# Optimization experiments

Measured on AMD Instinct MI355X. Metric: run time of the kernel, lower is better.

## Reference

```python
import jax, jax.numpy as jnp
import numpy as np

D_MODEL = 1024
N_SH = 16            # sub-heads per branch
N_BR = 4             # branches
H_TOT = N_BR * N_SH  # 64 total heads
DH = D_MODEL // N_SH # 64 head dim
BRANCH_CONFIGS = [(16, 0), (128, 16), (128, 0), (512, 144)]


def rms_norm(x):
    eps = jnp.finfo(x.dtype).eps
    return x * jax.lax.rsqrt(jnp.mean(x * x, axis=-1, keepdims=True) + eps)


def rope(x):
    # x: [B, H, T, Dh]; non-standard RoPE: even/odd split, halves concatenated
    T, Dh = x.shape[2], x.shape[3]
    inv_freq = 1.0 / (10000.0 ** (jnp.arange(0, Dh, 2, dtype=jnp.float32) / Dh))
    freqs = jnp.arange(T, dtype=jnp.float32)[:, None] * inv_freq[None, :]  # [T, Dh/2]
    cos = jnp.cos(freqs)[None, None]
    sin = jnp.sin(freqs)[None, None]
    x1 = x[..., 0::2]
    x2 = x[..., 1::2]
    return jnp.concatenate([-x2 * sin + x1 * cos, x1 * sin + x2 * cos], axis=-1)


def setup_inputs() -> dict:
    key = jax.random.key(0)
    ks = jax.random.split(key, 12)
    B, T, C = 2, 1024, D_MODEL
    s = 0.02
    return {
        "X": jax.random.normal(ks[0], (B, T, C), jnp.float32),
        "WQ": jax.random.normal(ks[1], (C, H_TOT * DH), jnp.float32) * s,
        "bQ": jax.random.normal(ks[2], (H_TOT * DH,), jnp.float32) * s,
        "WK": jax.random.normal(ks[3], (C, C), jnp.float32) * s,
        "bK": jax.random.normal(ks[4], (C,), jnp.float32) * s,
        "WV": jax.random.normal(ks[5], (C, H_TOT * DH), jnp.float32) * s,
        "bV": jax.random.normal(ks[6], (H_TOT * DH,), jnp.float32) * s,
        "WO": jax.random.normal(ks[7], (C, C), jnp.float32) * s,
        "bO": jax.random.normal(ks[8], (C,), jnp.float32) * s,
        "sink_scalars": jax.random.normal(ks[9], (H_TOT,), jnp.float32) * s,
        "v_nulls": jax.random.normal(ks[10], (H_TOT, DH), jnp.float32) * s,
    }


def reference(X, WQ, bQ, WK, bK, WV, bV, WO, bO, sink_scalars, v_nulls):
    B, T, C = X.shape
    # projections -> [B, H, T, Dh]
    q = (X @ WQ + bQ).reshape(B, T, H_TOT, DH).transpose(0, 2, 1, 3)
    q = rope(rms_norm(q))
    v = (X @ WV + bV).reshape(B, T, H_TOT, DH).transpose(0, 2, 1, 3)
    k = rope((X @ WK + bK).reshape(B, T, N_SH, DH).transpose(0, 2, 1, 3))
    k = jnp.tile(k, (1, N_BR, 1, 1))  # [B, H_TOT, T, Dh]

    # KMax scores with key self-norm denominator
    scores = jnp.einsum('bhqd,bhkd->bhqk', q, k)
    denom = jnp.sqrt(jnp.sum(k * k, axis=-1))[:, :, None, :]  # [B,H,1,T]
    w = scores / denom

    # banded masks per branch; note: off-band logits become 0 (NOT -inf) -> exp(0)=1 in softmax
    idx = jnp.arange(T)
    dist = idx[:, None] - idx[None, :]  # query - key
    bmasks = jnp.stack([((dist >= g) & (dist < h)).astype(w.dtype)
                        for (h, g) in BRANCH_CONFIGS], axis=0)  # [N_BR,T,T]
    full_mask = jnp.repeat(bmasks, N_SH, axis=0)[None]  # [1,H_TOT,T,T] (band subset of tril)
    w = w * full_mask

    # learnable tanh sink logit per head, concatenated as extra column
    sinks = jnp.broadcast_to(jnp.tanh(sink_scalars).reshape(1, H_TOT, 1, 1), (B, H_TOT, T, 1))
    probs = jax.nn.softmax(jnp.concatenate([w, sinks], axis=-1), axis=-1)

    out = jnp.einsum('bhqk,bhkd->bhqd', probs[..., :T], v)
    out = out + probs[..., T:] * v_nulls.reshape(1, H_TOT, 1, DH)

    # [B,H_TOT,T,Dh] -> [B,N_BR,T,C]
    ctx = out.reshape(B, N_BR, N_SH, T, DH).transpose(0, 1, 3, 2, 4).reshape(B, N_BR, T, C)
    y = ctx @ WO + bO
    return y.mean(axis=1)
```

## Files before the change

kernel.cpp:

```cpp
#include <hip/hip_runtime.h>
#include <hip/hip_bf16.h>
#include <math.h>

#define T_SEQ 1024
#define LOG2_10000 13.287712379549449f

typedef unsigned short u16;
typedef unsigned int u32;
typedef __attribute__((ext_vector_type(8))) short bf16x8;
typedef __attribute__((ext_vector_type(4))) float f32x4;

__device__ __forceinline__ void gload16(const u16* g, const u16* s) {
  __builtin_amdgcn_global_load_lds(
      (const __attribute__((address_space(1))) void*)g,
      (__attribute__((address_space(3))) void*)s, 16, 0, 0);
}

__device__ __forceinline__ u16 f2bf(float x) {
  __hip_bfloat16 h = __float2bfloat16(x);
  return *reinterpret_cast<u16*>(&h);
}
__device__ __forceinline__ float bf2f(u16 x) {
  __hip_bfloat16 h = *reinterpret_cast<__hip_bfloat16*>(&x);
  return __bfloat162float(h);
}

__device__ __forceinline__ float wave_sum64(float v) {
  v += __shfl_xor(v, 1, 64);
  v += __shfl_xor(v, 2, 64);
  v += __shfl_xor(v, 4, 64);
  v += __shfl_xor(v, 8, 64);
  v += __shfl_xor(v, 16, 64);
  v += __shfl_xor(v, 32, 64);
  return v;
}

__device__ __forceinline__ void transpose_step(
    const float* __restrict__ W, u16* __restrict__ Wt, int N, int nbx,
    int local, int t, float (*tile)[33]) {
  int bx = local % nbx, by = local / nbx;
  int n0 = bx * 32, k0 = by * 32;
  int r = t >> 3, c4 = (t & 7) * 4;
  float4 v = *reinterpret_cast<const float4*>(&W[(size_t)(k0 + r) * N + n0 + c4]);
  tile[r][c4 + 0] = v.x;
  tile[r][c4 + 1] = v.y;
  tile[r][c4 + 2] = v.z;
  tile[r][c4 + 3] = v.w;
  __syncthreads();
  u16 o[4];
#pragma unroll
  for (int i = 0; i < 4; ++i) o[i] = f2bf(tile[c4 + i][r]);
  *reinterpret_cast<uint2*>(&Wt[(size_t)(n0 + r) * 1024 + k0 + c4]) =
      *reinterpret_cast<const uint2*>(o);
}

__global__ __launch_bounds__(256) void prep_kernel(
    const float* __restrict__ X, const float* __restrict__ WQ,
    const float* __restrict__ WK, const float* __restrict__ WV,
    const float* __restrict__ WO, const float* __restrict__ bQ,
    const float* __restrict__ bV, const float* __restrict__ bK,
    u16* __restrict__ Xb, u16* __restrict__ WQVKt, u16* __restrict__ WOt,
    float* __restrict__ bQVK, float* __restrict__ ctab, float* __restrict__ stab)
{
  __shared__ float tile[32][33];
  const int blk = blockIdx.x, t = threadIdx.x;
  if (blk < 128) {
    int id = blk * 256 + t;
    int tt = id >> 5, p = id & 31;
    float invf = exp2f(-LOG2_10000 * (float)(2 * p) * (1.0f / 64.0f));
    float ang = (float)tt * invf;
    float sn, cs;
    sincosf(ang, &sn, &cs);
    ctab[id] = cs;
    stab[id] = sn;
  } else if (blk < 1152) {
    int i = (blk - 128) * 256 + t;
    float4 a = reinterpret_cast<const float4*>(X)[2 * i];
    float4 b = reinterpret_cast<const float4*>(X)[2 * i + 1];
    u16 o[8] = {f2bf(a.x), f2bf(a.y), f2bf(a.z), f2bf(a.w),
                f2bf(b.x), f2bf(b.y), f2bf(b.z), f2bf(b.w)};
    reinterpret_cast<uint4*>(Xb)[i] = *reinterpret_cast<const uint4*>(o);
  } else if (blk < 5248) {
    transpose_step(WQ, WQVKt, 4096, 128, blk - 1152, t, tile);
  } else if (blk < 9344) {
    transpose_step(WV, WQVKt + (size_t)4096 * 1024, 4096, 128, blk - 5248, t, tile);
  } else if (blk < 10368) {
    transpose_step(WK, WQVKt + (size_t)8192 * 1024, 1024, 32, blk - 9344, t, tile);
  } else if (blk < 11392) {
    transpose_step(WO, WOt, 1024, 32, blk - 10368, t, tile);
  } else {
    int id = (blk - 11392) * 256 + t;
    if (id < 9216)
      bQVK[id] = (id < 4096) ? bQ[id] : (id < 8192) ? bV[id - 4096] : bK[id - 8192];
  }
}

__global__ __launch_bounds__(256) void vsum_part_kernel(
    const u16* __restrict__ QVbf, float* __restrict__ part) {
  int blk = blockIdx.x;
  int b = blk >> 6, ch = blk & 63;
  const u16* base = QVbf + (size_t)(b * 1024 + ch * 16) * 8192 + 4096;
#pragma unroll
  for (int g = 0; g < 2; ++g) {
    int c0 = (threadIdx.x + g * 256) * 8;
    float s[8] = {0.f, 0.f, 0.f, 0.f, 0.f, 0.f, 0.f, 0.f};
#pragma unroll 4
    for (int r = 0; r < 16; ++r) {
      bf16x8 v = *reinterpret_cast<const bf16x8*>(&base[(size_t)r * 8192 + c0]);
#pragma unroll
      for (int e = 0; e < 8; ++e) s[e] += bf2f((u16)v[e]);
    }
    float* dst = &part[(size_t)blk * 4096 + c0];
#pragma unroll
    for (int e = 0; e < 8; ++e) dst[e] = s[e];
  }
}

__global__ __launch_bounds__(256) void vsum_reduce_kernel(
    const float* __restrict__ part, float* __restrict__ Vsum) {
  int id = blockIdx.x * 256 + threadIdx.x;
  int b = id >> 12, n = id & 4095;
  float s = 0.f;
#pragma unroll 8
  for (int ch = 0; ch < 64; ++ch) s += part[(size_t)(b * 64 + ch) * 4096 + n];
  Vsum[id] = s;
}

__global__ __launch_bounds__(512, 1) void gemm_qv_kernel(
    const u16* __restrict__ Ab, const u16* __restrict__ Bt,
    const float* __restrict__ bias, u16* __restrict__ Cqv)
{
  __shared__ __align__(16) u16 sA[4][256 * 32];
  __shared__ __align__(16) u16 sB[4][256 * 32];

  const int tid = threadIdx.x;
  const int lane = tid & 63;
  const int w = tid >> 6;
  const int wm = w >> 2, wn = w & 3;
  const int l15 = lane & 15, l4 = lane >> 4;

  const int orig = blockIdx.x;
  const int xcd = orig & 7, j = orig >> 3;
  const int by = (xcd >> 2) * 4 + (j >> 3);
  const int bx = (xcd & 3) * 8 + (j & 7);
  const int m0 = by * 256, n0 = bx * 256;

  const int r0s = tid >> 2,         c0s = tid & 3;
  const int r1s = (512 + tid) >> 2, c1s = (512 + tid) & 3;
  const int sc0 = c0s ^ ((r0s >> 1) & 3);
  const int sc1 = c1s ^ ((r1s >> 1) & 3);
  const u16* aA0 = Ab + (size_t)(m0 + r0s) * 1024 + 8 * sc0;
  const u16* aA1 = Ab + (size_t)(m0 + r1s) * 1024 + 8 * sc1;
  const u16* aB0 = Bt + (size_t)(n0 + r0s) * 1024 + 8 * sc0;
  const u16* aB1 = Bt + (size_t)(n0 + r1s) * 1024 + 8 * sc1;

  const int cp = l4 ^ ((l15 >> 1) & 3);

  f32x4 acc[8][4];
#pragma unroll
  for (int i = 0; i < 8; ++i)
#pragma unroll
    for (int jn = 0; jn < 4; ++jn) acc[i][jn] = (f32x4){0.f, 0.f, 0.f, 0.f};

#define STAGE32(t)                                                             \
  {                                                                            \
    const int sl = (t) & 3;                                                    \
    const int ko = (t) * 32;                                                   \
    gload16(aA0 + ko, &sA[sl][tid * 8]);                                       \
    gload16(aA1 + ko, &sA[sl][4096 + tid * 8]);                                \
    gload16(aB0 + ko, &sB[sl][tid * 8]);                                       \
    gload16(aB1 + ko, &sB[sl][4096 + tid * 8]);                                \
  }

  STAGE32(0);
  STAGE32(1);
#pragma unroll 1
  for (int t = 0; t < 32; ++t) {
    if (t + 2 < 32) {
      STAGE32(t + 2);
      asm volatile("s_waitcnt vmcnt(8)" ::: "memory");
    } else if (t + 1 < 32) {
      asm volatile("s_waitcnt vmcnt(4)" ::: "memory");
    } else {
      asm volatile("s_waitcnt vmcnt(0)" ::: "memory");
    }
    __builtin_amdgcn_sched_barrier(0);
    __builtin_amdgcn_s_barrier();
    __builtin_amdgcn_sched_barrier(0);

    const u16* tA = sA[t & 3];
    const u16* tB = sB[t & 3];

    bf16x8 bf[4];
#pragma unroll
    for (int n = 0; n < 4; ++n) {
      int row = wn * 64 + n * 16 + l15;
      bf[n] = *reinterpret_cast<const bf16x8*>(&tB[row * 32 + cp * 8]);
    }
    bf16x8 af[8];
#pragma unroll
    for (int m = 0; m < 8; ++m) {
      int row = wm * 128 + m * 16 + l15;
      af[m] = *reinterpret_cast<const bf16x8*>(&tA[row * 32 + cp * 8]);
    }
    __builtin_amdgcn_s_setprio(1);
#pragma unroll
    for (int m = 0; m < 8; ++m)
#pragma unroll
      for (int n = 0; n < 4; ++n)
        acc[m][n] = __builtin_amdgcn_mfma_f32_16x16x32_bf16(
            af[m], bf[n], acc[m][n], 0, 0, 0);
    __builtin_amdgcn_s_setprio(0);
  }
#undef STAGE32

#pragma unroll
  for (int n = 0; n < 4; ++n) {
    int col = n0 + wn * 64 + n * 16 + l15;
    float bv = bias[col];
#pragma unroll
    for (int mf = 0; mf < 8; ++mf) {
#pragma unroll
      for (int r = 0; r < 4; ++r) {
        int row = m0 + wm * 128 + mf * 16 + l4 * 4 + r;
        Cqv[(size_t)row * 8192 + col] = f2bf(acc[mf][n][r] + bv);
      }
    }
  }
}

template <bool BF16OUT>
__global__ __launch_bounds__(256) void gemm64_kernel(
    const u16* __restrict__ Ab, const u16* __restrict__ Bt,
    const float* __restrict__ bias, void* __restrict__ Cv,
    int M, int N, int K)
{
  __shared__ __align__(16) u16 sA[64 * 32];
  __shared__ __align__(16) u16 sB[64 * 32];
  const int tid = threadIdx.x;
  const int lane = tid & 63;
  const int wv = tid >> 6;
  const int wm = wv >> 1, wn = wv & 1;
  const int l15 = lane & 15, l4 = lane >> 4;
  const int m0 = blockIdx.y * 64, n0 = blockIdx.x * 64;

  f32x4 acc[2][2];
#pragma unroll
  for (int i = 0; i < 2; ++i)
#pragma unroll
    for (int j = 0; j < 2; ++j) acc[i][j] = (f32x4){0.f, 0.f, 0.f, 0.f};

  const int r0 = tid >> 2, kc = tid & 3;
  const u16* a_src = Ab + (size_t)(m0 + r0) * K + kc * 8;
  const u16* b_src = Bt + (size_t)(n0 + r0) * K + kc * 8;
  u16* dA = sA + (size_t)wv * 512;
  u16* dB = sB + (size_t)wv * 512;
  const int kcol = l4 * 8;

  for (int k0 = 0; k0 < K; k0 += 32) {
    __syncthreads();
    gload16(a_src + k0, dA);
    gload16(b_src + k0, dB);
    __syncthreads();
    bf16x8 af[2], bfv[2];
#pragma unroll
    for (int mi = 0; mi < 2; ++mi)
      af[mi] = *reinterpret_cast<const bf16x8*>(&sA[(wm * 32 + mi * 16 + l15) * 32 + kcol]);
#pragma unroll
    for (int ni = 0; ni < 2; ++ni)
      bfv[ni] = *reinterpret_cast<const bf16x8*>(&sB[(wn * 32 + ni * 16 + l15) * 32 + kcol]);
#pragma unroll
    for (int mi = 0; mi < 2; ++mi)
#pragma unroll
      for (int ni = 0; ni < 2; ++ni)
        acc[mi][ni] = __builtin_amdgcn_mfma_f32_16x16x32_bf16(
            af[mi], bfv[ni], acc[mi][ni], 0, 0, 0);
  }

#pragma unroll
  for (int mi = 0; mi < 2; ++mi)
#pragma unroll
    for (int ni = 0; ni < 2; ++ni) {
      int col = n0 + wn * 32 + ni * 16 + l15;
      float bv = bias[col];
#pragma unroll
      for (int r = 0; r < 4; ++r) {
        int row = m0 + wm * 32 + mi * 16 + l4 * 4 + r;
        float val = acc[mi][ni][r] + bv;
        size_t idx = (size_t)row * N + col;
        if (BF16OUT) ((u16*)Cv)[idx] = f2bf(val);
        else ((float*)Cv)[idx] = val;
      }
    }
}

__global__ __launch_bounds__(256) void qk_transform_kernel(
    u16* __restrict__ QVbf, u16* __restrict__ Kbf,
    const float* __restrict__ ctab, const float* __restrict__ stab)
{
  const int rid  = blockIdx.x * 8 + (threadIdx.x >> 5);
  const int lane = threadIdx.x & 63;
  const int p    = lane & 31;
  const int gb   = lane & 32;

  u16* row;
  int t;
  const bool isQ = rid < 131072;
  if (isQ) {
    int h = rid & 63, bt = rid >> 6;
    t = bt & 1023;
    row = QVbf + (size_t)bt * 8192 + h * 64;
  } else {
    int r2 = rid - 131072;
    int hsL = r2 & 15, bt = r2 >> 4;
    t = bt & 1023;
    row = Kbf + (size_t)bt * 1024 + hsL * 64;
  }

  u32 v = reinterpret_cast<const u32*>(row)[p];
  float x1 = bf2f((u16)v), x2 = bf2f((u16)(v >> 16));
  float cs = ctab[t * 32 + p], sn = stab[t * 32 + p];

  float o_lo, o_hi;
  if (isQ) {
    float ss = x1 * x1 + x2 * x2;
    ss += __shfl_xor(ss, 1, 64);
    ss += __shfl_xor(ss, 2, 64);
    ss += __shfl_xor(ss, 4, 64);
    ss += __shfl_xor(ss, 8, 64);
    ss += __shfl_xor(ss, 16, 64);
    float rs = rsqrtf(ss * (1.0f / 64.0f) + 1.1920929e-7f);
    float xn1 = x1 * rs, xn2 = x2 * rs;
    o_lo = xn1 * cs - xn2 * sn;
    o_hi = xn1 * sn + xn2 * cs;
  } else {
    float xr1 = x1 * cs - x2 * sn;
    float xr2 = x1 * sn + x2 * cs;
    float ss = xr1 * xr1 + xr2 * xr2;
    ss += __shfl_xor(ss, 1, 64);
    ss += __shfl_xor(ss, 2, 64);
    ss += __shfl_xor(ss, 4, 64);
    ss += __shfl_xor(ss, 8, 64);
    ss += __shfl_xor(ss, 16, 64);
    float rs = rsqrtf(ss);
    o_lo = xr1 * rs;
    o_hi = xr2 * rs;
  }

  int m = (2 * p) & 31;
  float slo0 = __shfl(o_lo, gb + m, 64);
  float slo1 = __shfl(o_lo, gb + m + 1, 64);
  float shi0 = __shfl(o_hi, gb + m, 64);
  float shi1 = __shfl(o_hi, gb + m + 1, 64);
  float e0 = (p < 16) ? slo0 : shi0;
  float e1 = (p < 16) ? slo1 : shi1;
  reinterpret_cast<u32*>(row)[p] = (u32)f2bf(e0) | ((u32)f2bf(e1) << 16);
}

__global__ __launch_bounds__(256) void attn_mfma_kernel(
    const u16* __restrict__ Qv, const u16* __restrict__ Kb,
    const float* __restrict__ Vsum, const float* __restrict__ sink,
    const float* __restrict__ vnull, u16* __restrict__ mctxb)
{
  __shared__ __align__(16) u16 sQ[64 * 64];
  __shared__ __align__(16) u16 sK[2][64 * 64];
  __shared__ __align__(16) u16 sVt[2][64 * 64];
  __shared__ __align__(16) u16 sP[64 * 64];

  int blk = blockIdx.x;
  blk = (blk & 7) * 64 + (blk >> 3);
  const int qt  = blk & 15;
  const int hs  = (blk >> 4) & 15;
  const int b   = blk >> 8;
  const int qt0 = qt * 64;

  const int tid  = threadIdx.x;
  const int lane = tid & 63;
  const int wv   = tid >> 6;
  const int l15  = lane & 15;
  const int l4   = lane >> 4;
  const int qr0  = tid >> 3, qi0 = tid & 7;
  const int qr1  = qr0 + 32;
  const int vjp  = tid & 31, vdg = tid >> 5;
  const int qrow = wv * 16 + l15;

  constexpr int HCFG[4] = {16, 128, 128, 512};
  constexpr int GCFG[4] = {0, 16, 0, 144};

  f32x4 macc[4];
#pragma unroll
  for (int i = 0; i < 4; ++i) macc[i] = (f32x4){0.f, 0.f, 0.f, 0.f};

#pragma unroll 1
  for (int br = 0; br < 4; ++br) {
    const int h = br * 16 + hs;
    const int hmax = HCFG[br], g = GCFG[br];
    int klo = qt0 - (hmax - 1); if (klo < 0) klo = 0;
    int khi = qt0 + 63 - g;     if (khi > 1023) khi = 1023;
    const int nc = (khi >= klo) ? ((khi - klo) / 64 + 1) : 0;

    gload16(Qv + (size_t)(b * 1024 + qt0 + qr0) * 8192 + h * 64 + 8 * (qi0 ^ (qr0 & 7)),
            sQ + (size_t)wv * 512);
    gload16(Qv + (size_t)(b * 1024 + qt0 + qr1) * 8192 + h * 64 + 8 * (qi0 ^ (qr1 & 7)),
            sQ + 2048 + (size_t)wv * 512);
    bf16x8 va, vb;
    if (nc > 0) {
      int ja0 = klo + qr0; if (ja0 > 1023) ja0 = 1023;
      int ja1 = klo + qr1; if (ja1 > 1023) ja1 = 1023;
      gload16(Kb + (size_t)(b * 1024 + ja0) * 1024 + hs * 64 + 8 * (qi0 ^ (qr0 & 7)),
              sK[0] + (size_t)wv * 512);
      gload16(Kb + (size_t)(b * 1024 + ja1) * 1024 + hs * 64 + 8 * (qi0 ^ (qr1 & 7)),
              sK[0] + 2048 + (size_t)wv * 512);
      int jva = klo + 2 * vjp, jvb = jva + 1;
      if (jva > 1023) jva = 1023;
      if (jvb > 1023) jvb = 1023;
      va = *reinterpret_cast<const bf16x8*>(
          &Qv[(size_t)(b * 1024 + jva) * 8192 + 4096 + h * 64 + vdg * 8]);
      vb = *reinterpret_cast<const bf16x8*>(
          &Qv[(size_t)(b * 1024 + jvb) * 8192 + 4096 + h * 64 + vdg * 8]);
    }
    asm volatile("s_waitcnt vmcnt(0)" ::: "memory");
    __builtin_amdgcn_sched_barrier(0);
    if (nc > 0) {
#pragma unroll
      for (int e = 0; e < 8; ++e) {
        int d = vdg * 8 + e;
        u32 pack = (u32)(u16)va[e] | ((u32)(u16)vb[e] << 16);
        *reinterpret_cast<u32*>(
            (char*)sVt[0] + d * 128 + ((4 * vjp) ^ ((d & 7) << 4))) = pack;
      }
    }
    asm volatile("s_waitcnt lgkmcnt(0)" ::: "memory");
    __builtin_amdgcn_sched_barrier(0);
    __builtin_amdgcn_s_barrier();

    bf16x8 afQ[2];
#pragma unroll
    for (int kh = 0; kh < 2; ++kh) {
      int cs = (4 * kh + l4) ^ (l15 & 7);
      afQ[kh] = *reinterpret_cast<const bf16x8*>(&sQ[qrow * 64 + cs * 8]);
    }

    f32x4 outv[4];
#pragma unroll
    for (int i = 0; i < 4; ++i) outv[i] = (f32x4){0.f, 0.f, 0.f, 0.f};
    float zacc[4] = {0.f, 0.f, 0.f, 0.f};

    int buf = 0;
#pragma unroll 1
    for (int c = 0; c < nc; ++c) {
      const int j0 = klo + c * 64;
      const bool nxt = (c + 1 < nc);
      if (nxt) {
        int j0n = j0 + 64;
        int ja0 = j0n + qr0; if (ja0 > 1023) ja0 = 1023;
        int ja1 = j0n + qr1; if (ja1 > 1023) ja1 = 1023;
        gload16(Kb + (size_t)(b * 1024 + ja0) * 1024 + hs * 64 + 8 * (qi0 ^ (qr0 & 7)),
                sK[buf ^ 1] + (size_t)wv * 512);
        gload16(Kb + (size_t)(b * 1024 + ja1) * 1024 + hs * 64 + 8 * (qi0 ^ (qr1 & 7)),
                sK[buf ^ 1] + 2048 + (size_t)wv * 512);
        int jva = j0n + 2 * vjp, jvb = jva + 1;
        if (jva > 1023) jva = 1023;
        if (jvb > 1023) jvb = 1023;
        va = *reinterpret_cast<const bf16x8*>(
            &Qv[(size_t)(b * 1024 + jva) * 8192 + 4096 + h * 64 + vdg * 8]);
        vb = *reinterpret_cast<const bf16x8*>(
            &Qv[(size_t)(b * 1024 + jvb) * 8192 + 4096 + h * 64 + vdg * 8]);
      }
      f32x4 sfr[4];
#pragma unroll
      for (int jt = 0; jt < 4; ++jt) {
        int krow = jt * 16 + l15;
        f32x4 acc = (f32x4){0.f, 0.f, 0.f, 0.f};
#pragma unroll
        for (int kh = 0; kh < 2; ++kh) {
          int cs = (4 * kh + l4) ^ (l15 & 7);
          bf16x8 bk = *reinterpret_cast<const bf16x8*>(&sK[buf][krow * 64 + cs * 8]);
          acc = __builtin_amdgcn_mfma_f32_16x16x32_bf16(afQ[kh], bk, acc, 0, 0, 0);
        }
        sfr[jt] = acc;
      }
#pragma unroll
      for (int jt = 0; jt < 4; ++jt) {
        int jloc = jt * 16 + l15;
        int jabs = j0 + jloc;
#pragma unroll
        for (int r = 0; r < 4; ++r) {
          int q_r = wv * 16 + l4 * 4 + r;
          int dist = (qt0 + q_r) - jabs;
          bool inband = (dist >= g) & (dist < hmax) & (jabs < 1024);
          float pv = inband ? (__expf(sfr[jt][r]) - 1.0f) : 0.0f;
          zacc[r] += pv;
          *reinterpret_cast<u16*>(
              (char*)sP + q_r * 128 + ((2 * jloc) ^ ((q_r & 7) << 4))) = f2bf(pv);
        }
      }
      asm volatile("s_waitcnt lgkmcnt(0)" ::: "memory");
      __builtin_amdgcn_sched_barrier(0);
      bf16x8 afP[2];
#pragma unroll
      for (int kh = 0; kh < 2; ++kh) {
        int cs = (4 * kh + l4) ^ (l15 & 7);
        afP[kh] = *reinterpret_cast<const bf16x8*>(&sP[qrow * 64 + cs * 8]);
      }
#pragma unroll
      for (int dt = 0; dt < 4; ++dt) {
        int drow = dt * 16 + l15;
#pragma unroll
        for (int kh = 0; kh < 2; ++kh) {
          int cs = (4 * kh + l4) ^ (l15 & 7);
          bf16x8 bv = *reinterpret_cast<const bf16x8*>(&sVt[buf][drow * 64 + cs * 8]);
          outv[dt] = __builtin_amdgcn_mfma_f32_16x16x32_bf16(afP[kh], bv, outv[dt], 0, 0, 0);
        }
      }
      if (nxt) {
#pragma unroll
        for (int e = 0; e < 8; ++e) {
          int d = vdg * 8 + e;
          u32 pack = (u32)(u16)va[e] | ((u32)(u16)vb[e] << 16);
          *reinterpret_cast<u32*>(
              (char*)sVt[buf ^ 1] + d * 128 + ((4 * vjp) ^ ((d & 7) << 4))) = pack;
        }
      }
      asm volatile("s_waitcnt vmcnt(0) lgkmcnt(0)" ::: "memory");
      __builtin_amdgcn_sched_barrier(0);
      __builtin_amdgcn_s_barrier();
      buf ^= 1;
    }

#pragma unroll
    for (int r = 0; r < 4; ++r) {
      zacc[r] += __shfl_xor(zacc[r], 1, 64);
      zacc[r] += __shfl_xor(zacc[r], 2, 64);
      zacc[r] += __shfl_xor(zacc[r], 4, 64);
      zacc[r] += __shfl_xor(zacc[r], 8, 64);
    }
    float es = __expf(tanhf(sink[h]));
#pragma unroll
    for (int dt = 0; dt < 4; ++dt) {
      int d = dt * 16 + l15;
      float vs = Vsum[(size_t)b * 4096 + h * 64 + d];
      float vn = vnull[h * 64 + d];
#pragma unroll
      for (int r = 0; r < 4; ++r) {
        float invZ = 1.0f / (1024.0f + zacc[r] + es);
        macc[dt][r] += (outv[dt][r] + vs + es * vn) * invZ;
      }
    }
  }

#pragma unroll
  for (int dt = 0; dt < 4; ++dt) {
#pragma unroll
    for (int r = 0; r < 4; ++r) {
      int q_r = wv * 16 + l4 * 4 + r;
      mctxb[(size_t)(b * 1024 + qt0 + q_r) * 1024 + hs * 64 + dt * 16 + l15] =
          f2bf(0.25f * macc[dt][r]);
    }
  }
}

extern "C" void kernel_launch(void* const* d_in, const int* in_sizes, int n_in,
                              void* d_out, int out_size, void* d_ws, size_t ws_size,
                              hipStream_t stream) {
  (void)in_sizes; (void)n_in; (void)out_size; (void)ws_size;
  const float* X    = (const float*)d_in[0];
  const float* WQ   = (const float*)d_in[1];
  const float* bQ   = (const float*)d_in[2];
  const float* WK   = (const float*)d_in[3];
  const float* bK   = (const float*)d_in[4];
  const float* WV   = (const float*)d_in[5];
  const float* bV   = (const float*)d_in[6];
  const float* WO   = (const float*)d_in[7];
  const float* bO   = (const float*)d_in[8];
  const float* sink = (const float*)d_in[9];
  const float* vnul = (const float*)d_in[10];
  float* Y = (float*)d_out;

  char* p = (char*)d_ws;
  u16*   Xb    = (u16*)p;   p += (size_t)2048 * 1024 * 2;
  u16*   WQVKt = (u16*)p;   p += (size_t)9216 * 1024 * 2;
  u16*   WOt   = (u16*)p;   p += (size_t)1024 * 1024 * 2;
  u16*   QVbf  = (u16*)p;   p += (size_t)2048 * 8192 * 2;
  u16*   Kbf   = (u16*)p;   p += (size_t)2048 * 1024 * 2;
  u16*   mctxb = (u16*)p;   p += (size_t)2048 * 1024 * 2;
  float* Vsum  = (float*)p; p += (size_t)2 * 4096 * 4;
  float* vpart = (float*)p; p += (size_t)128 * 4096 * 4;
  float* bQVK  = (float*)p; p += (size_t)9216 * 4;
  float* ctab  = (float*)p; p += (size_t)32768 * 4;
  float* stab  = (float*)p; p += (size_t)32768 * 4;

  dim3 blk(256);
  prep_kernel<<<11428, blk, 0, stream>>>(X, WQ, WK, WV, WO, bQ, bV, bK,
                                         Xb, WQVKt, WOt, bQVK, ctab, stab);

  gemm_qv_kernel<<<256, dim3(512), 0, stream>>>(Xb, WQVKt, bQVK, QVbf);
  gemm64_kernel<true><<<dim3(16, 32), blk, 0, stream>>>(
      Xb, WQVKt + (size_t)8192 * 1024, bQVK + 8192, Kbf, 2048, 1024, 1024);

  vsum_part_kernel<<<128, blk, 0, stream>>>(QVbf, vpart);
  vsum_reduce_kernel<<<32, blk, 0, stream>>>(vpart, Vsum);

  qk_transform_kernel<<<20480, blk, 0, stream>>>(QVbf, Kbf, ctab, stab);

  attn_mfma_kernel<<<512, blk, 0, stream>>>(QVbf, Kbf, Vsum, sink, vnul, mctxb);

  gemm64_kernel<false><<<dim3(16, 32), blk, 0, stream>>>(mctxb, WOt, bO, Y, 2048, 1024, 1024);
}
```

Before: 139.7 us.

## Fuse Q RMSNorm+RoPE into QV GEMM epilogue and double-buffer gemm64

Q normalization and rotary embedding move into the QV GEMM epilogue, computed from accumulators with lane shuffles, so the standalone transform now handles only K rows. This avoids a separate read-modify-write pass over the 2048x4096 bf16 Q region. The small 64x64 GEMM also gains a double-buffered LDS pipeline, prefetching the next K-slice while computing the current one. The cost is a heavier epilogue with extra shuffles and table loads, plus reliance on manual waitcnt/barrier ordering.

```diff
diff --git a/kernel.cpp b/kernel.cpp
--- a/kernel.cpp
+++ b/kernel.cpp
@@ -23,16 +23,6 @@
 __device__ __forceinline__ float bf2f(u16 x) {
   __hip_bfloat16 h = *reinterpret_cast<__hip_bfloat16*>(&x);
   return __bfloat162float(h);
-}
-
-__device__ __forceinline__ float wave_sum64(float v) {
-  v += __shfl_xor(v, 1, 64);
-  v += __shfl_xor(v, 2, 64);
-  v += __shfl_xor(v, 4, 64);
-  v += __shfl_xor(v, 8, 64);
-  v += __shfl_xor(v, 16, 64);
-  v += __shfl_xor(v, 32, 64);
-  return v;
 }
 
 __device__ __forceinline__ void transpose_step(
@@ -128,7 +118,8 @@
 
 __global__ __launch_bounds__(512, 1) void gemm_qv_kernel(
     const u16* __restrict__ Ab, const u16* __restrict__ Bt,
-    const float* __restrict__ bias, u16* __restrict__ Cqv)
+    const float* __restrict__ bias, u16* __restrict__ Cqv,
+    const float* __restrict__ ctab, const float* __restrict__ stab)
 {
   __shared__ __align__(16) u16 sA[4][256 * 32];
   __shared__ __align__(16) u16 sB[4][256 * 32];
@@ -214,16 +205,60 @@
   }
 #undef STAGE32
 
-#pragma unroll
-  for (int n = 0; n < 4; ++n) {
-    int col = n0 + wn * 64 + n * 16 + l15;
-    float bv = bias[col];
+  float bv4[4];
+#pragma unroll
+  for (int n = 0; n < 4; ++n) bv4[n] = bias[n0 + wn * 64 + n * 16 + l15];
+
+  if (bx < 16) {
+    const int srcl = (lane & 0x30) | ((2 * l15) & 15);
+    const bool hi8 = (l15 >= 8);
 #pragma unroll
     for (int mf = 0; mf < 8; ++mf) {
 #pragma unroll
       for (int r = 0; r < 4; ++r) {
         int row = m0 + wm * 128 + mf * 16 + l4 * 4 + r;
-        Cqv[(size_t)row * 8192 + col] = f2bf(acc[mf][n][r] + bv);
+        int tt = row & 1023;
+        float v0 = acc[mf][0][r] + bv4[0];
+        float v1 = acc[mf][1][r] + bv4[1];
+        float v2 = acc[mf][2][r] + bv4[2];
+        float v3 = acc[mf][3][r] + bv4[3];
+        float ss = v0 * v0 + v1 * v1 + v2 * v2 + v3 * v3;
+        ss += __shfl_xor(ss, 1, 64);
+        ss += __shfl_xor(ss, 2, 64);
+        ss += __shfl_xor(ss, 4, 64);
+        ss += __shfl_xor(ss, 8, 64);
+        float rs = rsqrtf(ss * (1.0f / 64.0f) + 1.1920929e-7f);
+        float x0 = v0 * rs, x1f = v1 * rs, x2f = v2 * rs, x3f = v3 * rs;
+        float tc0 = ctab[tt * 32 + l15],      ts0 = stab[tt * 32 + l15];
+        float tc1 = ctab[tt * 32 + 16 + l15], ts1 = stab[tt * 32 + 16 + l15];
+        float e0a = __shfl(x0,  srcl, 64),     e0b = __shfl(x1f, srcl, 64);
+        float o0a = __shfl(x0,  srcl + 1, 64), o0b = __shfl(x1f, srcl + 1, 64);
+        float e1a = __shfl(x2f, srcl, 64),     e1b = __shfl(x3f, srcl, 64);
+        float o1a = __shfl(x2f, srcl + 1, 64), o1b = __shfl(x3f, srcl + 1, 64);
+        float X1_0 = hi8 ? e0b : e0a, X2_0 = hi8 ? o0b : o0a;
+        float X1_1 = hi8 ? e1b : e1a, X2_1 = hi8 ? o1b : o1a;
+        u16 out0 = f2bf(X1_0 * tc0 - X2_0 * ts0);
+        u16 out1 = f2bf(X1_1 * tc1 - X2_1 * ts1);
+        u16 out2 = f2bf(X1_0 * ts0 + X2_0 * tc0);
+        u16 out3 = f2bf(X1_1 * ts1 + X2_1 * tc1);
+        size_t base_ = (size_t)row * 8192 + n0 + wn * 64 + l15;
+        Cqv[base_ + 0]  = out0;
+        Cqv[base_ + 16] = out1;
+        Cqv[base_ + 32] = out2;
+        Cqv[base_ + 48] = out3;
+      }
+    }
+  } else {
+#pragma unroll
+    for (int n = 0; n < 4; ++n) {
+      int col = n0 + wn * 64 + n * 16 + l15;
+#pragma unroll
+      for (int mf = 0; mf < 8; ++mf) {
+#pragma unroll
+        for (int r = 0; r < 4; ++r) {
+          int row = m0 + wm * 128 + mf * 16 + l4 * 4 + r;
+          Cqv[(size_t)row * 8192 + col] = f2bf(acc[mf][n][r] + bv4[n]);
+        }
       }
     }
   }
@@ -235,8 +270,8 @@
     const float* __restrict__ bias, void* __restrict__ Cv,
     int M, int N, int K)
 {
-  __shared__ __align__(16) u16 sA[64 * 32];
-  __shared__ __align__(16) u16 sB[64 * 32];
+  __shared__ __align__(16) u16 sA[2][64 * 32];
+  __shared__ __align__(16) u16 sB[2][64 * 32];
   const int tid = threadIdx.x;
   const int lane = tid & 63;
   const int wv = tid >> 6;
@@ -253,22 +288,33 @@
   const int r0 = tid >> 2, kc = tid & 3;
   const u16* a_src = Ab + (size_t)(m0 + r0) * K + kc * 8;
   const u16* b_src = Bt + (size_t)(n0 + r0) * K + kc * 8;
-  u16* dA = sA + (size_t)wv * 512;
-  u16* dB = sB + (size_t)wv * 512;
   const int kcol = l4 * 8;
 
-  for (int k0 = 0; k0 < K; k0 += 32) {
-    __syncthreads();
-    gload16(a_src + k0, dA);
-    gload16(b_src + k0, dB);
-    __syncthreads();
+  gload16(a_src, &sA[0][(size_t)wv * 512]);
+  gload16(b_src, &sB[0][(size_t)wv * 512]);
+
+  const int niter = K >> 5;
+#pragma unroll 1
+  for (int it = 0; it < niter; ++it) {
+    const int buf = it & 1;
+    __builtin_amdgcn_s_barrier();
+    if (it + 1 < niter) {
+      gload16(a_src + (it + 1) * 32, &sA[buf ^ 1][(size_t)wv * 512]);
+      gload16(b_src + (it + 1) * 32, &sB[buf ^ 1][(size_t)wv * 512]);
+      asm volatile("s_waitcnt vmcnt(2)" ::: "memory");
+    } else {
+      asm volatile("s_waitcnt vmcnt(0)" ::: "memory");
+    }
+    __builtin_amdgcn_sched_barrier(0);
     bf16x8 af[2], bfv[2];
 #pragma unroll
     for (int mi = 0; mi < 2; ++mi)
-      af[mi] = *reinterpret_cast<const bf16x8*>(&sA[(wm * 32 + mi * 16 + l15) * 32 + kcol]);
+      af[mi] = *reinterpret_cast<const bf16x8*>(
+          &sA[buf][(wm * 32 + mi * 16 + l15) * 32 + kcol]);
 #pragma unroll
     for (int ni = 0; ni < 2; ++ni)
-      bfv[ni] = *reinterpret_cast<const bf16x8*>(&sB[(wn * 32 + ni * 16 + l15) * 32 + kcol]);
+      bfv[ni] = *reinterpret_cast<const bf16x8*>(
+          &sB[buf][(wn * 32 + ni * 16 + l15) * 32 + kcol]);
 #pragma unroll
     for (int mi = 0; mi < 2; ++mi)
 #pragma unroll
@@ -294,58 +340,33 @@
     }
 }
 
-__global__ __launch_bounds__(256) void qk_transform_kernel(
-    u16* __restrict__ QVbf, u16* __restrict__ Kbf,
-    const float* __restrict__ ctab, const float* __restrict__ stab)
+__global__ __launch_bounds__(256) void k_transform_kernel(
+    u16* __restrict__ Kbf, const float* __restrict__ ctab,
+    const float* __restrict__ stab)
 {
   const int rid  = blockIdx.x * 8 + (threadIdx.x >> 5);
   const int lane = threadIdx.x & 63;
   const int p    = lane & 31;
   const int gb   = lane & 32;
 
-  u16* row;
-  int t;
-  const bool isQ = rid < 131072;
-  if (isQ) {
-    int h = rid & 63, bt = rid >> 6;
-    t = bt & 1023;
-    row = QVbf + (size_t)bt * 8192 + h * 64;
-  } else {
-    int r2 = rid - 131072;
-    int hsL = r2 & 15, bt = r2 >> 4;
-    t = bt & 1023;
-    row = Kbf + (size_t)bt * 1024 + hsL * 64;
-  }
+  int hsL = rid & 15, bt = rid >> 4, t = bt & 1023;
+  u16* row = Kbf + (size_t)bt * 1024 + hsL * 64;
 
   u32 v = reinterpret_cast<const u32*>(row)[p];
   float x1 = bf2f((u16)v), x2 = bf2f((u16)(v >> 16));
   float cs = ctab[t * 32 + p], sn = stab[t * 32 + p];
 
-  float o_lo, o_hi;
-  if (isQ) {
-    float ss = x1 * x1 + x2 * x2;
-    ss += __shfl_xor(ss, 1, 64);
-    ss += __shfl_xor(ss, 2, 64);
-    ss += __shfl_xor(ss, 4, 64);
-    ss += __shfl_xor(ss, 8, 64);
-    ss += __shfl_xor(ss, 16, 64);
-    float rs = rsqrtf(ss * (1.0f / 64.0f) + 1.1920929e-7f);
-    float xn1 = x1 * rs, xn2 = x2 * rs;
-    o_lo = xn1 * cs - xn2 * sn;
-    o_hi = xn1 * sn + xn2 * cs;
-  } else {
-    float xr1 = x1 * cs - x2 * sn;
-    float xr2 = x1 * sn + x2 * cs;
-    float ss = xr1 * xr1 + xr2 * xr2;
-    ss += __shfl_xor(ss, 1, 64);
-    ss += __shfl_xor(ss, 2, 64);
-    ss += __shfl_xor(ss, 4, 64);
-    ss += __shfl_xor(ss, 8, 64);
-    ss += __shfl_xor(ss, 16, 64);
-    float rs = rsqrtf(ss);
-    o_lo = xr1 * rs;
-    o_hi = xr2 * rs;
-  }
+  float xr1 = x1 * cs - x2 * sn;
+  float xr2 = x1 * sn + x2 * cs;
+  float ss = xr1 * xr1 + xr2 * xr2;
+  ss += __shfl_xor(ss, 1, 64);
+  ss += __shfl_xor(ss, 2, 64);
+  ss += __shfl_xor(ss, 4, 64);
+  ss += __shfl_xor(ss, 8, 64);
+  ss += __shfl_xor(ss, 16, 64);
+  float rs = rsqrtf(ss);
+  float o_lo = xr1 * rs;
+  float o_hi = xr2 * rs;
 
   int m = (2 * p) & 31;
   float slo0 = __shfl(o_lo, gb + m, 64);
@@ -594,14 +615,14 @@
   prep_kernel<<<11428, blk, 0, stream>>>(X, WQ, WK, WV, WO, bQ, bV, bK,
                                          Xb, WQVKt, WOt, bQVK, ctab, stab);
 
-  gemm_qv_kernel<<<256, dim3(512), 0, stream>>>(Xb, WQVKt, bQVK, QVbf);
+  gemm_qv_kernel<<<256, dim3(512), 0, stream>>>(Xb, WQVKt, bQVK, QVbf, ctab, stab);
   gemm64_kernel<true><<<dim3(16, 32), blk, 0, stream>>>(
       Xb, WQVKt + (size_t)8192 * 1024, bQVK + 8192, Kbf, 2048, 1024, 1024);
 
   vsum_part_kernel<<<128, blk, 0, stream>>>(QVbf, vpart);
   vsum_reduce_kernel<<<32, blk, 0, stream>>>(vpart, Vsum);
 
-  qk_transform_kernel<<<20480, blk, 0, stream>>>(QVbf, Kbf, ctab, stab);
+  k_transform_kernel<<<4096, blk, 0, stream>>>(Kbf, ctab, stab);
 
   attn_mfma_kernel<<<512, blk, 0, stream>>>(QVbf, Kbf, Vsum, sink, vnul, mctxb);
 
```

New measurement: 137.6 us. About the same (-1.5%).

## Double-buffer swizzled gemm64 tiles and fuse vsum partials into qk transform

Applied to the files above, without the earlier changes.

The 64x64 GEMM used for the K and output projections now loads K=64 slabs into double-buffered, XOR-swizzled LDS. The next slab is prefetched while the current one is computed, with a waitcnt-based handoff instead of two full barriers per 32-wide step. The V column partial-sum blocks are appended to the QK rotary/normalization launch as extra blocks, which removes one kernel launch. This doubles LDS use per block and relies on hand-placed waitcnt ordering.

```diff
diff --git a/kernel.cpp b/kernel.cpp
--- a/kernel.cpp
+++ b/kernel.cpp
@@ -23,16 +23,6 @@
 __device__ __forceinline__ float bf2f(u16 x) {
   __hip_bfloat16 h = *reinterpret_cast<__hip_bfloat16*>(&x);
   return __bfloat162float(h);
-}
-
-__device__ __forceinline__ float wave_sum64(float v) {
-  v += __shfl_xor(v, 1, 64);
-  v += __shfl_xor(v, 2, 64);
-  v += __shfl_xor(v, 4, 64);
-  v += __shfl_xor(v, 8, 64);
-  v += __shfl_xor(v, 16, 64);
-  v += __shfl_xor(v, 32, 64);
-  return v;
 }
 
 __device__ __forceinline__ void transpose_step(
@@ -95,37 +85,6 @@
   }
 }
 
-__global__ __launch_bounds__(256) void vsum_part_kernel(
-    const u16* __restrict__ QVbf, float* __restrict__ part) {
-  int blk = blockIdx.x;
-  int b = blk >> 6, ch = blk & 63;
-  const u16* base = QVbf + (size_t)(b * 1024 + ch * 16) * 8192 + 4096;
-#pragma unroll
-  for (int g = 0; g < 2; ++g) {
-    int c0 = (threadIdx.x + g * 256) * 8;
-    float s[8] = {0.f, 0.f, 0.f, 0.f, 0.f, 0.f, 0.f, 0.f};
-#pragma unroll 4
-    for (int r = 0; r < 16; ++r) {
-      bf16x8 v = *reinterpret_cast<const bf16x8*>(&base[(size_t)r * 8192 + c0]);
-#pragma unroll
-      for (int e = 0; e < 8; ++e) s[e] += bf2f((u16)v[e]);
-    }
-    float* dst = &part[(size_t)blk * 4096 + c0];
-#pragma unroll
-    for (int e = 0; e < 8; ++e) dst[e] = s[e];
-  }
-}
-
-__global__ __launch_bounds__(256) void vsum_reduce_kernel(
-    const float* __restrict__ part, float* __restrict__ Vsum) {
-  int id = blockIdx.x * 256 + threadIdx.x;
-  int b = id >> 12, n = id & 4095;
-  float s = 0.f;
-#pragma unroll 8
-  for (int ch = 0; ch < 64; ++ch) s += part[(size_t)(b * 64 + ch) * 4096 + n];
-  Vsum[id] = s;
-}
-
 __global__ __launch_bounds__(512, 1) void gemm_qv_kernel(
     const u16* __restrict__ Ab, const u16* __restrict__ Bt,
     const float* __restrict__ bias, u16* __restrict__ Cqv)
@@ -235,8 +194,8 @@
     const float* __restrict__ bias, void* __restrict__ Cv,
     int M, int N, int K)
 {
-  __shared__ __align__(16) u16 sA[64 * 32];
-  __shared__ __align__(16) u16 sB[64 * 32];
+  __shared__ __align__(16) u16 sA[2][64 * 64];
+  __shared__ __align__(16) u16 sB[2][64 * 64];
   const int tid = threadIdx.x;
   const int lane = tid & 63;
   const int wv = tid >> 6;
@@ -250,31 +209,60 @@
 #pragma unroll
     for (int j = 0; j < 2; ++j) acc[i][j] = (f32x4){0.f, 0.f, 0.f, 0.f};
 
-  const int r0 = tid >> 2, kc = tid & 3;
-  const u16* a_src = Ab + (size_t)(m0 + r0) * K + kc * 8;
-  const u16* b_src = Bt + (size_t)(n0 + r0) * K + kc * 8;
-  u16* dA = sA + (size_t)wv * 512;
-  u16* dB = sB + (size_t)wv * 512;
-  const int kcol = l4 * 8;
-
-  for (int k0 = 0; k0 < K; k0 += 32) {
-    __syncthreads();
-    gload16(a_src + k0, dA);
-    gload16(b_src + k0, dB);
-    __syncthreads();
-    bf16x8 af[2], bfv[2];
-#pragma unroll
-    for (int mi = 0; mi < 2; ++mi)
-      af[mi] = *reinterpret_cast<const bf16x8*>(&sA[(wm * 32 + mi * 16 + l15) * 32 + kcol]);
-#pragma unroll
-    for (int ni = 0; ni < 2; ++ni)
-      bfv[ni] = *reinterpret_cast<const bf16x8*>(&sB[(wn * 32 + ni * 16 + l15) * 32 + kcol]);
-#pragma unroll
-    for (int mi = 0; mi < 2; ++mi)
-#pragma unroll
-      for (int ni = 0; ni < 2; ++ni)
-        acc[mi][ni] = __builtin_amdgcn_mfma_f32_16x16x32_bf16(
-            af[mi], bfv[ni], acc[mi][ni], 0, 0, 0);
+  const int r0s = tid >> 3,         c0s = tid & 7;
+  const int r1s = (256 + tid) >> 3, c1s = (256 + tid) & 7;
+  const int sc0 = c0s ^ (r0s & 7);
+  const int sc1 = c1s ^ (r1s & 7);
+  const u16* aA0 = Ab + (size_t)(m0 + r0s) * K + 8 * sc0;
+  const u16* aA1 = Ab + (size_t)(m0 + r1s) * K + 8 * sc1;
+  const u16* aB0 = Bt + (size_t)(n0 + r0s) * K + 8 * sc0;
+  const u16* aB1 = Bt + (size_t)(n0 + r1s) * K + 8 * sc1;
+
+  gload16(aA0, &sA[0][tid * 8]);
+  gload16(aA1, &sA[0][2048 + tid * 8]);
+  gload16(aB0, &sB[0][tid * 8]);
+  gload16(aB1, &sB[0][2048 + tid * 8]);
+
+  const int niter = K >> 6;
+#pragma unroll 1
+  for (int it = 0; it < niter; ++it) {
+    const int buf = it & 1;
+    __builtin_amdgcn_s_barrier();
+    if (it + 1 < niter) {
+      const int ko = (it + 1) * 64;
+      gload16(aA0 + ko, &sA[buf ^ 1][tid * 8]);
+      gload16(aA1 + ko, &sA[buf ^ 1][2048 + tid * 8]);
+      gload16(aB0 + ko, &sB[buf ^ 1][tid * 8]);
+      gload16(aB1 + ko, &sB[buf ^ 1][2048 + tid * 8]);
+      asm volatile("s_waitcnt vmcnt(4)" ::: "memory");
+    } else {
+      asm volatile("s_waitcnt vmcnt(0)" ::: "memory");
+    }
+    __builtin_amdgcn_sched_barrier(0);
+    bf16x8 af[2][2], bfv[2][2];
+#pragma unroll
+    for (int kk = 0; kk < 2; ++kk) {
+#pragma unroll
+      for (int mi = 0; mi < 2; ++mi) {
+        int row = wm * 32 + mi * 16 + l15;
+        int cs = (kk * 4 + l4) ^ (row & 7);
+        af[mi][kk] = *reinterpret_cast<const bf16x8*>(&sA[buf][row * 64 + cs * 8]);
+      }
+#pragma unroll
+      for (int ni = 0; ni < 2; ++ni) {
+        int row = wn * 32 + ni * 16 + l15;
+        int cs = (kk * 4 + l4) ^ (row & 7);
+        bfv[ni][kk] = *reinterpret_cast<const bf16x8*>(&sB[buf][row * 64 + cs * 8]);
+      }
+    }
+#pragma unroll
+    for (int kk = 0; kk < 2; ++kk)
+#pragma unroll
+      for (int mi = 0; mi < 2; ++mi)
+#pragma unroll
+        for (int ni = 0; ni < 2; ++ni)
+          acc[mi][ni] = __builtin_amdgcn_mfma_f32_16x16x32_bf16(
+              af[mi][kk], bfv[ni][kk], acc[mi][ni], 0, 0, 0);
   }
 
 #pragma unroll
@@ -294,67 +282,99 @@
     }
 }
 
-__global__ __launch_bounds__(256) void qk_transform_kernel(
+__global__ __launch_bounds__(256) void qkvt_kernel(
     u16* __restrict__ QVbf, u16* __restrict__ Kbf,
-    const float* __restrict__ ctab, const float* __restrict__ stab)
+    const float* __restrict__ ctab, const float* __restrict__ stab,
+    float* __restrict__ part)
 {
-  const int rid  = blockIdx.x * 8 + (threadIdx.x >> 5);
-  const int lane = threadIdx.x & 63;
-  const int p    = lane & 31;
-  const int gb   = lane & 32;
-
-  u16* row;
-  int t;
-  const bool isQ = rid < 131072;
-  if (isQ) {
-    int h = rid & 63, bt = rid >> 6;
-    t = bt & 1023;
-    row = QVbf + (size_t)bt * 8192 + h * 64;
+  const int blk = blockIdx.x;
+  if (blk < 20480) {
+    const int rid  = blk * 8 + (threadIdx.x >> 5);
+    const int lane = threadIdx.x & 63;
+    const int p    = lane & 31;
+    const int gb   = lane & 32;
+
+    u16* row;
+    int t;
+    const bool isQ = rid < 131072;
+    if (isQ) {
+      int h = rid & 63, bt = rid >> 6;
+      t = bt & 1023;
+      row = QVbf + (size_t)bt * 8192 + h * 64;
+    } else {
+      int r2 = rid - 131072;
+      int hsL = r2 & 15, bt = r2 >> 4;
+      t = bt & 1023;
+      row = Kbf + (size_t)bt * 1024 + hsL * 64;
+    }
+
+    u32 v = reinterpret_cast<const u32*>(row)[p];
+    float x1 = bf2f((u16)v), x2 = bf2f((u16)(v >> 16));
+    float cs = ctab[t * 32 + p], sn = stab[t * 32 + p];
+
+    float o_lo, o_hi;
+    if (isQ) {
+      float ss = x1 * x1 + x2 * x2;
+      ss += __shfl_xor(ss, 1, 64);
+      ss += __shfl_xor(ss, 2, 64);
+      ss += __shfl_xor(ss, 4, 64);
+      ss += __shfl_xor(ss, 8, 64);
+      ss += __shfl_xor(ss, 16, 64);
+      float rs = rsqrtf(ss * (1.0f / 64.0f) + 1.1920929e-7f);
+      float xn1 = x1 * rs, xn2 = x2 * rs;
+      o_lo = xn1 * cs - xn2 * sn;
+      o_hi = xn1 * sn + xn2 * cs;
+    } else {
+      float xr1 = x1 * cs - x2 * sn;
+      float xr2 = x1 * sn + x2 * cs;
+      float ss = xr1 * xr1 + xr2 * xr2;
+      ss += __shfl_xor(ss, 1, 64);
+      ss += __shfl_xor(ss, 2, 64);
+      ss += __shfl_xor(ss, 4, 64);
+      ss += __shfl_xor(ss, 8, 64);
+      ss += __shfl_xor(ss, 16, 64);
+      float rs = rsqrtf(ss);
+      o_lo = xr1 * rs;
+      o_hi = xr2 * rs;
+    }
+
+    int m = (2 * p) & 31;
+    float slo0 = __shfl(o_lo, gb + m, 64);
+    float slo1 = __shfl(o_lo, gb + m + 1, 64);
+    float shi0 = __shfl(o_hi, gb + m, 64);
+    float shi1 = __shfl(o_hi, gb + m + 1, 64);
+    float e0 = (p < 16) ? slo0 : shi0;
+    float e1 = (p < 16) ? slo1 : shi1;
+    reinterpret_cast<u32*>(row)[p] = (u32)f2bf(e0) | ((u32)f2bf(e1) << 16);
   } else {
-    int r2 = rid - 131072;
-    int hsL = r2 & 15, bt = r2 >> 4;
-    t = bt & 1023;
-    row = Kbf + (size_t)bt * 1024 + hsL * 64;
-  }
-
-  u32 v = reinterpret_cast<const u32*>(row)[p];
-  float x1 = bf2f((u16)v), x2 = bf2f((u16)(v >> 16));
-  float cs = ctab[t * 32 + p], sn = stab[t * 32 + p];
-
-  float o_lo, o_hi;
-  if (isQ) {
-    float ss = x1 * x1 + x2 * x2;
-    ss += __shfl_xor(ss, 1, 64);
-    ss += __shfl_xor(ss, 2, 64);
-    ss += __shfl_xor(ss, 4, 64);
-    ss += __shfl_xor(ss, 8, 64);
-    ss += __shfl_xor(ss, 16, 64);
-    float rs = rsqrtf(ss * (1.0f / 64.0f) + 1.1920929e-7f);
-    float xn1 = x1 * rs, xn2 = x2 * rs;
-    o_lo = xn1 * cs - xn2 * sn;
-    o_hi = xn1 * sn + xn2 * cs;
-  } else {
-    float xr1 = x1 * cs - x2 * sn;
-    float xr2 = x1 * sn + x2 * cs;
-    float ss = xr1 * xr1 + xr2 * xr2;
-    ss += __shfl_xor(ss, 1, 64);
-    ss += __shfl_xor(ss, 2, 64);
-    ss += __shfl_xor(ss, 4, 64);
-    ss += __shfl_xor(ss, 8, 64);
-    ss += __shfl_xor(ss, 16, 64);
-    float rs = rsqrtf(ss);
-    o_lo = xr1 * rs;
-    o_hi = xr2 * rs;
-  }
-
-  int m = (2 * p) & 31;
-  float slo0 = __shfl(o_lo, gb + m, 64);
-  float slo1 = __shfl(o_lo, gb + m + 1, 64);
-  float shi0 = __shfl(o_hi, gb + m, 64);
-  float shi1 = __shfl(o_hi, gb + m + 1, 64);
-  float e0 = (p < 16) ? slo0 : shi0;
-  float e1 = (p < 16) ? slo1 : shi1;
-  reinterpret_cast<u32*>(row)[p] = (u32)f2bf(e0) | ((u32)f2bf(e1) << 16);
+    int vb = blk - 20480;
+    int b = vb >> 6, ch = vb & 63;
+    const u16* base = QVbf + (size_t)(b * 1024 + ch * 16) * 8192 + 4096;
+#pragma unroll
+    for (int g = 0; g < 2; ++g) {
+      int c0 = (threadIdx.x + g * 256) * 8;
+      float s[8] = {0.f, 0.f, 0.f, 0.f, 0.f, 0.f, 0.f, 0.f};
+#pragma unroll 4
+      for (int r = 0; r < 16; ++r) {
+        bf16x8 v = *reinterpret_cast<const bf16x8*>(&base[(size_t)r * 8192 + c0]);
+#pragma unroll
+        for (int e = 0; e < 8; ++e) s[e] += bf2f((u16)v[e]);
+      }
+      float* dst = &part[(size_t)vb * 4096 + c0];
+#pragma unroll
+      for (int e = 0; e < 8; ++e) dst[e] = s[e];
+    }
+  }
+}
+
+__global__ __launch_bounds__(256) void vsum_reduce_kernel(
+    const float* __restrict__ part, float* __restrict__ Vsum) {
+  int id = blockIdx.x * 256 + threadIdx.x;
+  int b = id >> 12, n = id & 4095;
+  float s = 0.f;
+#pragma unroll 8
+  for (int ch = 0; ch < 64; ++ch) s += part[(size_t)(b * 64 + ch) * 4096 + n];
+  Vsum[id] = s;
 }
 
 __global__ __launch_bounds__(256) void attn_mfma_kernel(
@@ -598,11 +618,9 @@
   gemm64_kernel<true><<<dim3(16, 32), blk, 0, stream>>>(
       Xb, WQVKt + (size_t)8192 * 1024, bQVK + 8192, Kbf, 2048, 1024, 1024);
 
-  vsum_part_kernel<<<128, blk, 0, stream>>>(QVbf, vpart);
+  qkvt_kernel<<<20608, blk, 0, stream>>>(QVbf, Kbf, ctab, stab, vpart);
   vsum_reduce_kernel<<<32, blk, 0, stream>>>(vpart, Vsum);
 
-  qk_transform_kernel<<<20480, blk, 0, stream>>>(QVbf, Kbf, ctab, stab);
-
   attn_mfma_kernel<<<512, blk, 0, stream>>>(QVbf, Kbf, Vsum, sink, vnul, mctxb);
 
   gemm64_kernel<false><<<dim3(16, 32), blk, 0, stream>>>(mctxb, WOt, bO, Y, 2048, 1024, 1024);
```

Result: faster. 132.7 us (-5.0%).
